# Performance work log

Hardware: AMD Instinct MI355X
Metric: run time of the kernel (lower is better)

The kernel has to match this reference:

```python
import jax, jax.numpy as jnp
import numpy as np

WS = 16      # window_size
OWS = 24     # overlap_win_size = int(16*0.5) + 16
PAD = 4      # (OWS - WS) // 2
NH = 6       # num_heads
DIM = 192
MLP_HID = 384  # dim * mlp_ratio(2)
TABLE = (WS + OWS - 1) ** 2  # 1521


def _ln(x, g, b, eps=1e-5):
    m = x.mean(-1, keepdims=True)
    v = ((x - m) ** 2).mean(-1, keepdims=True)
    return (x - m) * jax.lax.rsqrt(v + eps) * g + b


def setup_inputs() -> dict:
    key = jax.random.key(0)
    ks = jax.random.split(key, 16)
    B, H, W, C = 1, 192, 192, DIM
    x = jax.random.normal(ks[0], (B, H * W, C), jnp.float32)
    rpi = jax.random.randint(ks[1], (WS * WS, OWS * OWS), 0, TABLE, dtype=jnp.int64)
    s = 0.02
    return {
        "x": x,
        "rpi": rpi,
        "h": H,
        "w": W,
        "norm1_g": jnp.ones((C,), jnp.float32),
        "norm1_b": jnp.zeros((C,), jnp.float32),
        "qkv_w": jax.random.normal(ks[2], (C, 3 * C), jnp.float32) * s,
        "qkv_b": jnp.zeros((3 * C,), jnp.float32),
        "rpb_table": jax.random.normal(ks[3], (TABLE, NH), jnp.float32) * s,
        "proj_w": jax.random.normal(ks[4], (C, C), jnp.float32) * s,
        "proj_b": jnp.zeros((C,), jnp.float32),
        "norm2_g": jnp.ones((C,), jnp.float32),
        "norm2_b": jnp.zeros((C,), jnp.float32),
        "fc1_w": jax.random.normal(ks[5], (C, MLP_HID), jnp.float32) * s,
        "fc1_b": jnp.zeros((MLP_HID,), jnp.float32),
        "fc2_w": jax.random.normal(ks[6], (MLP_HID, C), jnp.float32) * s,
        "fc2_b": jnp.zeros((C,), jnp.float32),
    }


def reference(x, rpi, h, w, norm1_g, norm1_b, qkv_w, qkv_b, rpb_table,
              proj_w, proj_b, norm2_g, norm2_b, fc1_w, fc1_b, fc2_w, fc2_b):
    B, L, C = x.shape
    d = C // NH
    scale = d ** -0.5
    nhw, nww = h // WS, w // WS
    nW = nhw * nww

    shortcut = x
    xn = _ln(x, norm1_g, norm1_b).reshape(B, h, w, C)
    qkv = xn @ qkv_w + qkv_b                       # (B, h, w, 3C)
    q, k, v = jnp.split(qkv, 3, axis=-1)

    # non-overlapping query windows: (B*nW, WS*WS, C)
    qw = q.reshape(B, nhw, WS, nww, WS, C).transpose(0, 1, 3, 2, 4, 5)
    qw = qw.reshape(B * nW, WS * WS, C)

    # overlapping key/value windows via padded gather (equiv. to nn.Unfold)
    ri = (jnp.arange(nhw) * WS)[:, None] + jnp.arange(OWS)[None, :]  # (nhw, OWS)
    ci = (jnp.arange(nww) * WS)[:, None] + jnp.arange(OWS)[None, :]  # (nww, OWS)

    def win(t):
        tp = jnp.pad(t, ((0, 0), (PAD, PAD), (PAD, PAD), (0, 0)))
        g = tp[:, ri[:, :, None, None], ci[None, None, :, :], :]     # (B,nhw,OWS,nww,OWS,C)
        return g.transpose(0, 1, 3, 2, 4, 5).reshape(B * nW, OWS * OWS, C)

    kw, vw = win(k), win(v)

    qh = qw.reshape(B * nW, WS * WS, NH, d).transpose(0, 2, 1, 3) * scale
    kh = kw.reshape(B * nW, OWS * OWS, NH, d).transpose(0, 2, 1, 3)
    vh = vw.reshape(B * nW, OWS * OWS, NH, d).transpose(0, 2, 1, 3)

    attn = jnp.einsum('bhqd,bhkd->bhqk', qh, kh)
    bias = rpb_table[rpi.reshape(-1)].reshape(WS * WS, OWS * OWS, NH)
    bias = bias.transpose(2, 0, 1)                 # (NH, nq, n)
    attn = jax.nn.softmax(attn + bias[None], axis=-1)
    out = jnp.einsum('bhqk,bhkd->bhqd', attn, vh)
    out = out.transpose(0, 2, 1, 3).reshape(B * nW, WS * WS, C)

    # window reverse
    xr = out.reshape(B, nhw, nww, WS, WS, C).transpose(0, 1, 3, 2, 4, 5)
    xr = xr.reshape(B, h * w, C)

    x2 = xr @ proj_w + proj_b + shortcut
    x3 = _ln(x2, norm2_g, norm2_b)
    mlp = jax.nn.gelu(x3 @ fc1_w + fc1_b, approximate=False) @ fc2_w + fc2_b
    return x2 + mlp
```

## Files before the change

### kernel.cpp

```cpp
#include <hip/hip_runtime.h>
#include <hip/hip_bf16.h>

#define NH 6
#define DIM 192
#define HW 192
#define M_TOK (HW*HW)
#define QSC 0.25503488f
#define L2E 1.4426950408889634f

typedef __attribute__((ext_vector_type(8))) __bf16 bf16x8;
typedef __attribute__((ext_vector_type(8))) short short8;
typedef __attribute__((ext_vector_type(4))) short s16x4;
typedef __attribute__((ext_vector_type(4))) float floatx4;

__device__ inline unsigned short f2bf(float f) {
    union { float f; unsigned int u; } v; v.f = f;
    unsigned int r = (v.u + 0x7FFFu + ((v.u >> 16) & 1u)) >> 16;
    return (unsigned short)r;
}
__device__ inline short f2bfh(float f) {
    __bf16 b = (__bf16)f;
    return __builtin_bit_cast(short, b);
}
__device__ inline float exp2fast(float x) {
#if __has_builtin(__builtin_amdgcn_exp2f)
    return __builtin_amdgcn_exp2f(x);
#else
    return exp2f(x);
#endif
}
__device__ inline floatx4 bf4f(s16x4 b) {
    floatx4 f;
    #pragma unroll
    for (int r = 0; r < 4; r++) {
        union { unsigned u; float f; } v;
        v.u = ((unsigned)(unsigned short)b[r]) << 16;
        f[r] = v.f;
    }
    return f;
}

__device__ inline floatx4 mfma16(short8 a, short8 b, floatx4 c) {
    return __builtin_amdgcn_mfma_f32_16x16x32_bf16(
        __builtin_bit_cast(bf16x8, a), __builtin_bit_cast(bf16x8, b), c, 0, 0, 0);
}

template <int OFF>
__device__ inline s16x4 tr16(unsigned addr) {
    s16x4 r;
    asm volatile("ds_read_b64_tr_b16 %0, %1 offset:%2"
                 : "=&v"(r) : "v"(addr), "i"(OFF));
    return r;
}
template <int OFF>
__device__ inline s16x4 tr16m(unsigned addr) {
    s16x4 r;
    asm volatile("ds_read_b64_tr_b16 %0, %1 offset:%2"
                 : "=&v"(r) : "v"(addr), "i"(OFF) : "memory");
    return r;
}
template <int N>
__device__ __forceinline__ void wait_lgkm() {
    asm volatile("s_waitcnt lgkmcnt(%0)" :: "i"(N) : "memory");
}
__device__ inline short8 cat8(s16x4 a, s16x4 b) {
    return __builtin_shufflevector(a, b, 0, 1, 2, 3, 4, 5, 6, 7);
}

__device__ __forceinline__ void gload16(const void* g, unsigned lds_off) {
    __builtin_amdgcn_global_load_lds(
        (const __attribute__((address_space(1))) unsigned int*)(uintptr_t)g,
        (__attribute__((address_space(3))) unsigned int*)(uintptr_t)lds_off,
        16, 0, 0);
}

__device__ __forceinline__ void btfrag_body(int id, const int* __restrict__ rpi,
                                            const float* __restrict__ table,
                                            unsigned short* __restrict__ btf) {
    int lane = id & 63;
    int t = id >> 6;
    int kt = t % 36; t /= 36;
    int qt = t & 15; int hh = t >> 4;
    int k = kt * 16 + (lane & 15);
    int qb = qt * 16 + (lane >> 4) * 4;
    s16x4 v;
    #pragma unroll
    for (int r = 0; r < 4; r++)
        v[r] = f2bfh(table[rpi[(qb + r) * 576 + k] * NH + hh] * L2E);
    *(s16x4*)&btf[(size_t)id * 4] = v;
}

__device__ __forceinline__ void wcast_rest_body(int i2, const float* __restrict__ projw,
                                                const float* __restrict__ fc1w,
                                                const float* __restrict__ fc2w,
                                                unsigned short* __restrict__ wt_proj,
                                                unsigned short* __restrict__ wt_fc1,
                                                unsigned short* __restrict__ wt_fc2) {
    if (i2 < 36864) {
        int n = i2 / 192, k = i2 - n * 192;
        wt_proj[i2] = f2bf(projw[k * 192 + n]);
    } else if (i2 < 110592) {
        int i = i2 - 36864;
        int n = i / 192, k = i - n * 192;
        wt_fc1[i] = f2bf(fc1w[k * 384 + n]);
    } else {
        int i = i2 - 110592;
        int n = i / 384, k = i - n * 384;
        wt_fc2[i] = f2bf(fc2w[k * 192 + n]);
    }
}

__global__ __launch_bounds__(256) void prep_kernel(
    const float* __restrict__ qkvw,
    const float* __restrict__ x, const float* __restrict__ n1g,
    const float* __restrict__ n1b,
    unsigned short* __restrict__ wt_qkv,
    unsigned short* __restrict__ xn) {
    int bid = blockIdx.x;
    if (bid < 432) {
        int id = bid * 256 + threadIdx.x;
        int n = id / 192, k = id - n * 192;
        wt_qkv[id] = f2bf(qkvw[k * 576 + n]);
    } else {
        int row = (bid - 432) * 4 + (threadIdx.x >> 6);
        int lane = threadIdx.x & 63;
        const float* r = x + (size_t)row * DIM;
        float x0 = r[lane], x1 = r[lane + 64], x2 = r[lane + 128];
        float s = x0 + x1 + x2;
        #pragma unroll
        for (int m = 32; m >= 1; m >>= 1) s += __shfl_xor(s, m);
        float mean = s * (1.f / 192.f);
        float d0 = x0 - mean, d1 = x1 - mean, d2 = x2 - mean;
        float v = d0 * d0 + d1 * d1 + d2 * d2;
        #pragma unroll
        for (int m = 32; m >= 1; m >>= 1) v += __shfl_xor(v, m);
        float rstd = rsqrtf(v * (1.f / 192.f) + 1e-5f);
        unsigned short* o = xn + (size_t)row * DIM;
        o[lane]       = f2bf(d0 * rstd * n1g[lane]       + n1b[lane]);
        o[lane + 64]  = f2bf(d1 * rstd * n1g[lane + 64]  + n1b[lane + 64]);
        o[lane + 128] = f2bf(d2 * rstd * n1g[lane + 128] + n1b[lane + 128]);
    }
}

template <int MODE, int KK>
__global__ __launch_bounds__(256, 4) void gemm_kernel(
    const unsigned short* __restrict__ A,
    const unsigned short* __restrict__ Wt,
    const float* __restrict__ bias,
    void* __restrict__ outp,
    int N,
    const int* __restrict__ rpi, const float* __restrict__ table,
    unsigned short* __restrict__ btf,
    const float* __restrict__ projw, const float* __restrict__ fc1w,
    const float* __restrict__ fc2w,
    unsigned short* __restrict__ wt_proj, unsigned short* __restrict__ wt_fc1,
    unsigned short* __restrict__ wt_fc2) {
    if (MODE == 0 && blockIdx.y >= 9) {
        int extra = (blockIdx.y - 9) * 288 + blockIdx.x;
        if (extra < 864) {
            btfrag_body(extra * 256 + threadIdx.x, rpi, table, btf);
        } else if (extra < 1584) {
            wcast_rest_body((extra - 864) * 256 + threadIdx.x,
                            projw, fc1w, fc2w, wt_proj, wt_fc1, wt_fc2);
        }
        return;
    }
    __shared__ __align__(16) short sAB[19968];
    constexpr int STAGES = KK / 96;
    int tid = threadIdx.x;
    int w = tid >> 6, lane = tid & 63;
    int bm = blockIdx.x, bn = blockIdx.y;
    int lr = lane & 15, h = lane >> 4;
    floatx4 acc[2][4];
    #pragma unroll
    for (int i = 0; i < 2; i++)
        #pragma unroll
        for (int j = 0; j < 4; j++) acc[i][j] = (floatx4){0.f, 0.f, 0.f, 0.f};

    unsigned ldsbase = (unsigned)(uintptr_t)&sAB[0];

    for (int s = 0; s < STAGES; s++) {
        if (s) __syncthreads();
        for (int W = w; W < 39; W += 4) {
            int o = W * 1024 + lane * 16;
            const unsigned short* src;
            if (o < 26624) {
                int r = o / 208;
                int c = (o - r * 208) >> 4; c = c < 12 ? c : 11;
                src = &A[(size_t)(bm * 128 + r) * KK + s * 96 + c * 8];
            } else {
                int o2 = o - 26624;
                int r = o2 / 208;
                int c = (o2 - r * 208) >> 4; c = c < 12 ? c : 11;
                src = &Wt[(size_t)(bn * 64 + r) * KK + s * 96 + c * 8];
            }
            gload16(src, ldsbase + (unsigned)(W * 1024));
        }
        __syncthreads();
        #pragma unroll
        for (int kk = 0; kk < 3; kk++) {
            int kc = (kk * 4 + h) * 8;
            short8 a0 = *(const short8*)&sAB[(w * 32 + lr) * 104 + kc];
            short8 a1 = *(const short8*)&sAB[(w * 32 + 16 + lr) * 104 + kc];
            short8 b0 = *(const short8*)&sAB[13312 + (lr) * 104 + kc];
            short8 b1 = *(const short8*)&sAB[13312 + (16 + lr) * 104 + kc];
            short8 b2 = *(const short8*)&sAB[13312 + (32 + lr) * 104 + kc];
            short8 b3 = *(const short8*)&sAB[13312 + (48 + lr) * 104 + kc];
            acc[0][0] = mfma16(a0, b0, acc[0][0]);
            acc[0][1] = mfma16(a0, b1, acc[0][1]);
            acc[0][2] = mfma16(a0, b2, acc[0][2]);
            acc[0][3] = mfma16(a0, b3, acc[0][3]);
            acc[1][0] = mfma16(a1, b0, acc[1][0]);
            acc[1][1] = mfma16(a1, b1, acc[1][1]);
            acc[1][2] = mfma16(a1, b2, acc[1][2]);
            acc[1][3] = mfma16(a1, b3, acc[1][3]);
        }
    }

    int rowbase = bm * 128 + w * 32 + h * 4;
    int colbase = bn * 64;
    #pragma unroll
    for (int mi = 0; mi < 2; mi++) {
        #pragma unroll
        for (int ni = 0; ni < 4; ni++) {
            int c = colbase + ni * 16 + lr;
            float bv = bias[c];
            #pragma unroll
            for (int j = 0; j < 4; j++) {
                int r = rowbase + mi * 16 + j;
                float v = acc[mi][ni][j] + bv;
                if (MODE == 0) {
                    int part = c / 192;
                    int rem = c - part * 192;
                    int hd = rem >> 5, d = rem & 31;
                    if (part == 0) v *= QSC;
                    ((unsigned short*)outp)[((size_t)(part * 6 + hd) * M_TOK + r) * 32 + d] = f2bf(v);
                }
            }
        }
    }
}

__global__ __launch_bounds__(256, 2) void mega_kernel(
    const unsigned short* __restrict__ Aop,
    const unsigned short* __restrict__ Wp,
    const unsigned short* __restrict__ W1,
    const unsigned short* __restrict__ W2,
    const float* __restrict__ pb,
    const float* __restrict__ b1,
    const float* __restrict__ b2f,
    const float* __restrict__ res,
    const float* __restrict__ g2, const float* __restrict__ bb2,
    float* __restrict__ outp) {
    __shared__ __align__(16) short sA[13312];
    __shared__ __align__(16) short sH[6656];
    __shared__ __align__(16) short sB[10240];
    int tid = threadIdx.x;
    int w = tid >> 6, lane = tid & 63;
    int bm = blockIdx.x;
    int lr = lane & 15, h = lane >> 4;
    int lrow0 = w * 16 + h * 4;
    int row0 = bm * 64 + lrow0;

    floatx4 x2a[12];
    #pragma unroll
    for (int t = 0; t < 12; t++) x2a[t] = (floatx4){0.f, 0.f, 0.f, 0.f};

    auto stageB = [&](const unsigned short* base, int stride) {
        unsigned ldsB = (unsigned)(uintptr_t)&sB[0];
        #pragma unroll
        for (int W = 0; W < 5; W++) {
            int Wc = W * 4 + w;
            int o = Wc * 1024 + lane * 16;
            int r = o / 208;
            int c = (o - r * 208) >> 4; c = c < 12 ? c : 11;
            if (r > 95) { r = 95; c = 11; }
            gload16(&base[r * stride + c * 8], ldsB + (unsigned)(Wc * 1024));
        }
    };

    {
        unsigned ldsA = (unsigned)(uintptr_t)&sA[0];
        for (int W = w; W < 26; W += 4) {
            int o = W * 1024 + lane * 16;
            int sl = o / 13312;
            int o2 = o - sl * 13312;
            int r = o2 / 208;
            int c = (o2 - r * 208) >> 4; c = c < 12 ? c : 11;
            int col = sl * 96 + c * 8;
            int hd = col >> 5, d = col & 31;
            gload16(&Aop[((size_t)hd * M_TOK + bm * 64 + r) * 32 + d],
                    ldsA + (unsigned)(W * 1024));
        }
    }

#define GEMM6(ACCBASE, SAPTR) { \
    _Pragma("unroll") for (int kk = 0; kk < 3; kk++) { int kc = (kk * 4 + h) * 8; \
        short8 a_ = *(const short8*)&(SAPTR)[(w * 16 + lr) * 104 + kc]; \
        _Pragma("unroll") for (int ni = 0; ni < 6; ni++) { \
            short8 b_ = *(const short8*)&sB[(ni * 16 + lr) * 104 + kc]; \
            x2a[(ACCBASE) + ni] = mfma16(a_, b_, x2a[(ACCBASE) + ni]); } } }

#define GEMMH(SAPTR) { \
    _Pragma("unroll") for (int kk = 0; kk < 3; kk++) { int kc = (kk * 4 + h) * 8; \
        short8 a_ = *(const short8*)&(SAPTR)[(w * 16 + lr) * 104 + kc]; \
        _Pragma("unroll") for (int ni = 0; ni < 6; ni++) { \
            short8 b_ = *(const short8*)&sB[(ni * 16 + lr) * 104 + kc]; \
            ha[ni] = mfma16(a_, b_, ha[ni]); } } }

    stageB(Wp, 192);
    __syncthreads();
    GEMM6(0, sA);
    __syncthreads(); stageB(Wp + 96, 192); __syncthreads();
    GEMM6(0, sA + 6656);
    __syncthreads(); stageB(Wp + 96 * 192, 192); __syncthreads();
    GEMM6(6, sA);
    __syncthreads(); stageB(Wp + 96 * 192 + 96, 192); __syncthreads();
    GEMM6(6, sA + 6656);

    {
        float s1[4] = {0.f, 0.f, 0.f, 0.f}, s2[4] = {0.f, 0.f, 0.f, 0.f};
        #pragma unroll
        for (int t = 0; t < 12; t++) {
            int c = t * 16 + lr;
            float bv = pb[c];
            #pragma unroll
            for (int j = 0; j < 4; j++) {
                size_t idx = (size_t)(row0 + j) * 192 + c;
                float v = x2a[t][j] + bv + res[idx];
                x2a[t][j] = v;
                s1[j] += v;
                s2[j] += v * v;
            }
        }
        #pragma unroll
        for (int mask = 1; mask <= 8; mask <<= 1) {
            #pragma unroll
            for (int j = 0; j < 4; j++) {
                s1[j] += __shfl_xor(s1[j], mask);
                s2[j] += __shfl_xor(s2[j], mask);
            }
        }
        float mean[4], rstd[4];
        #pragma unroll
        for (int j = 0; j < 4; j++) {
            mean[j] = s1[j] * (1.f / 192.f);
            float var = s2[j] * (1.f / 192.f) - mean[j] * mean[j];
            rstd[j] = rsqrtf(var + 1e-5f);
        }
        #pragma unroll
        for (int t = 0; t < 12; t++) {
            int c = t * 16 + lr;
            float gw = g2[c], bw = bb2[c];
            int slab = t / 6;
            int cc = c - slab * 96;
            #pragma unroll
            for (int j = 0; j < 4; j++) {
                float lnv = (x2a[t][j] - mean[j]) * rstd[j] * gw + bw;
                sA[slab * 6656 + (lrow0 + j) * 104 + cc] = f2bfh(lnv);
            }
        }
    }

    for (int q = 0; q < 4; q++) {
        floatx4 ha[6];
        #pragma unroll
        for (int ni = 0; ni < 6; ni++) ha[ni] = (floatx4){0.f, 0.f, 0.f, 0.f};

        __syncthreads(); stageB(W1 + (size_t)(q * 96) * 192, 192); __syncthreads();
        GEMMH(sA);
        __syncthreads(); stageB(W1 + (size_t)(q * 96) * 192 + 96, 192); __syncthreads();
        GEMMH(sA + 6656);

        #pragma unroll
        for (int ni = 0; ni < 6; ni++) {
            int c384 = q * 96 + ni * 16 + lr;
            float bv = b1[c384];
            #pragma unroll
            for (int j = 0; j < 4; j++) {
                float v = ha[ni][j] + bv;
                float gl = 0.5f * v * (1.f + erff(v * 0.70710678118654752f));
                sH[(lrow0 + j) * 104 + ni * 16 + lr] = f2bfh(gl);
            }
        }

        __syncthreads(); stageB(W2 + q * 96, 384); __syncthreads();
        GEMM6(0, sH);
        __syncthreads(); stageB(W2 + (size_t)96 * 384 + q * 96, 384); __syncthreads();
        GEMM6(6, sH);
    }
#undef GEMM6
#undef GEMMH

    #pragma unroll
    for (int t = 0; t < 12; t++) {
        int c = t * 16 + lr;
        float bv = b2f[c];
        #pragma unroll
        for (int j = 0; j < 4; j++) {
            size_t idx = (size_t)(row0 + j) * 192 + c;
            outp[idx] = x2a[t][j] + bv;
        }
    }
}

__global__ __launch_bounds__(256, 3) void attn_mfma_kernel(
    const unsigned short* __restrict__ qkv,
    const unsigned short* __restrict__ btf,
    unsigned short* __restrict__ out) {
    __shared__ __align__(16) short sK[2][2304];
    __shared__ __align__(16) short sV[2][2048];
    __shared__ __align__(16) short sPt[4][4096];
    int win = blockIdx.x, head = blockIdx.y;
    int iy = win / 12, ix = win % 12;
    int tid = threadIdx.x;
    int w = tid >> 6, lane = tid & 63;
    int m = lane & 15, h = lane >> 4;

    const unsigned short* Qp = qkv + (size_t)head * M_TOK * 32;
    const unsigned short* Kp = qkv + (size_t)(6 + head) * M_TOK * 32;

    short8 qf[4];
    #pragma unroll
    for (int i = 0; i < 4; i++) {
        int wy = w * 4 + i;
        size_t tok = (size_t)(iy * 16 + wy) * HW + ix * 16 + m;
        qf[i] = *(const short8*)&Qp[tok * 32 + h * 8];
    }

    short ob = (m == 0) ? (short)0x3F80 : (short)0;
    short8 bones = {ob, ob, ob, ob, ob, ob, ob, ob};

    floatx4 oacc[4][2];
    floatx4 lacc[4];
    #pragma unroll
    for (int i = 0; i < 4; i++) {
        lacc[i] = (floatx4){0.f, 0.f, 0.f, 0.f};
        oacc[i][0] = (floatx4){0.f, 0.f, 0.f, 0.f};
        oacc[i][1] = (floatx4){0.f, 0.f, 0.f, 0.f};
    }

    int skey = tid >> 2, dq = tid & 3;
    short* kdst = &sK[0][skey * 36 + dq * 8];
    short* vdst = &sV[0][(dq >> 1) * 1024 + (skey >> 2) * 64 + (skey & 3) * 16 + (dq & 1) * 8];

    auto fetch = [&](int c, short8& kv, short8& vv) {
        int key = c * 64 + skey;
        int oy = key / 24, ox = key - (key / 24) * 24;
        int gy = iy * 16 - 4 + oy, gx = ix * 16 - 4 + ox;
        kv = (short8){0,0,0,0,0,0,0,0};
        vv = (short8){0,0,0,0,0,0,0,0};
        if (gy >= 0 && gy < HW && gx >= 0 && gx < HW) {
            const unsigned short* p = &Kp[((size_t)gy * HW + gx) * 32 + dq * 8];
            kv = *(const short8*)p;
            vv = *(const short8*)(p + 6 * M_TOK * 32);
        }
    };

    {
        short8 kv, vv;
        fetch(0, kv, vv);
        *(short8*)kdst = kv;
        *(short8*)vdst = vv;
    }

    unsigned sPbase = (unsigned)(uintptr_t)&sPt[w][0];
    unsigned sPa = sPbase + 8 * m + 256 * h;
    unsigned sVa0 = (unsigned)(uintptr_t)&sV[0][0] + 8 * m + 256 * h;
    char* sPwb = (char*)&sPt[w][0] + 128 * (m >> 2) + 32 * (m & 3) + 8 * h;

    for (int c = 0; c < 9; c++) {
        __syncthreads();
        int cur = c & 1;
        short8 knx, vnx;
        bool more = (c < 8);
        if (more) fetch(c + 1, knx, vnx);

        const short* sKc = sK[cur];
        short8 kfrag[4];
        #pragma unroll
        for (int kt = 0; kt < 4; kt++)
            kfrag[kt] = *(const short8*)&sKc[(kt * 16 + m) * 36 + h * 8];

        const unsigned short* bb = btf + ((((size_t)head * 16 + w * 4) * 36 + c * 4) * 64 + lane) * 4;

        #pragma unroll
        for (int i = 0; i < 4; i++) {
            floatx4 s[4];
            #pragma unroll
            for (int kt = 0; kt < 4; kt++)
                s[kt] = bf4f(*(const s16x4*)&bb[(size_t)(i * 36 + kt) * 256]);
            #pragma unroll
            for (int kt = 0; kt < 4; kt++)
                s[kt] = mfma16(qf[i], kfrag[kt], s[kt]);
            #pragma unroll
            for (int kt = 0; kt < 4; kt++) {
                s16x4 pk;
                #pragma unroll
                for (int r = 0; r < 4; r++)
                    pk[r] = f2bfh(exp2fast(s[kt][r]));
                *(s16x4*)(sPwb + i * 2048 + kt * 512) = pk;
            }
        }

        unsigned sVa = sVa0 + cur * 4096;
        short8 vb[4];
        {
            s16x4 lo0 = tr16<0>(sVa),    hi0 = tr16<128>(sVa);
            s16x4 lo1 = tr16<2048>(sVa), hi1 = tr16<2176>(sVa);
            s16x4 lo2 = tr16<1024>(sVa), hi2 = tr16<1152>(sVa);
            s16x4 lo3 = tr16<3072>(sVa), hi3 = tr16<3200>(sVa);
            vb[0] = cat8(lo0, hi0);
            vb[1] = cat8(lo1, hi1);
            vb[2] = cat8(lo2, hi2);
            vb[3] = cat8(lo3, hi3);
        }
        s16x4 pl0 = tr16m<0>(sPa),    ph0 = tr16m<128>(sPa);
        s16x4 pl1 = tr16m<1024>(sPa), ph1 = tr16m<1152>(sPa);
        #pragma unroll
        for (int i = 0; i < 4; i++) {
            s16x4 nl0, nh0, nl1, nh1;
            if (i < 3) {
                unsigned a = sPa + (unsigned)((i + 1) * 2048);
                nl0 = tr16m<0>(a);    nh0 = tr16m<128>(a);
                nl1 = tr16m<1024>(a); nh1 = tr16m<1152>(a);
                wait_lgkm<4>();
            } else {
                wait_lgkm<0>();
            }
            __builtin_amdgcn_sched_barrier(0);
            short8 pa0 = cat8(pl0, ph0);
            short8 pa1 = cat8(pl1, ph1);
            oacc[i][0] = mfma16(pa0, vb[0], oacc[i][0]);
            oacc[i][1] = mfma16(pa0, vb[1], oacc[i][1]);
            oacc[i][0] = mfma16(pa1, vb[2], oacc[i][0]);
            oacc[i][1] = mfma16(pa1, vb[3], oacc[i][1]);
            lacc[i] = mfma16(pa0, bones, lacc[i]);
            lacc[i] = mfma16(pa1, bones, lacc[i]);
            if (i < 3) { pl0 = nl0; ph0 = nh0; pl1 = nl1; ph1 = nh1; }
        }

        if (more) {
            int nb = 1 - cur;
            *(short8*)(kdst + nb * 2304) = knx;
            *(short8*)(vdst + nb * 2048) = vnx;
        }
    }

    unsigned short* Op = out + (size_t)head * M_TOK * 32;
    #pragma unroll
    for (int i = 0; i < 4; i++) {
        float inv[4];
        #pragma unroll
        for (int r = 0; r < 4; r++) {
            float sum = __shfl(lacc[i][r], lane & 48);
            inv[r] = 1.f / sum;
        }
        int wy = w * 4 + i;
        #pragma unroll
        for (int dt = 0; dt < 2; dt++)
            #pragma unroll
            for (int r = 0; r < 4; r++) {
                size_t tok = (size_t)(iy * 16 + wy) * HW + ix * 16 + h * 4 + r;
                Op[tok * 32 + dt * 16 + m] = f2bf(oacc[i][dt][r] * inv[r]);
            }
    }
}

extern "C" void kernel_launch(void* const* d_in, const int* in_sizes, int n_in,
                              void* d_out, int out_size, void* d_ws, size_t ws_size,
                              hipStream_t stream) {
    const float* x     = (const float*)d_in[0];
    const int*   rpi   = (const int*)d_in[1];
    const float* n1g   = (const float*)d_in[4];
    const float* n1b   = (const float*)d_in[5];
    const float* qkvw  = (const float*)d_in[6];
    const float* qkvb  = (const float*)d_in[7];
    const float* rpb   = (const float*)d_in[8];
    const float* projw = (const float*)d_in[9];
    const float* projb = (const float*)d_in[10];
    const float* n2g   = (const float*)d_in[11];
    const float* n2b   = (const float*)d_in[12];
    const float* fc1w  = (const float*)d_in[13];
    const float* fc1b  = (const float*)d_in[14];
    const float* fc2w  = (const float*)d_in[15];
    const float* fc2b  = (const float*)d_in[16];

    char* ws = (char*)d_ws;
    unsigned short* wt_qkv  = (unsigned short*)ws;
    unsigned short* wt_proj = wt_qkv + 110592;
    unsigned short* wt_fc1  = wt_proj + 36864;
    unsigned short* wt_fc2  = wt_fc1 + 73728;
    unsigned short* btf     = (unsigned short*)(ws + 589824);
    unsigned short* xn      = (unsigned short*)(ws + 4128768);
    unsigned short* qkv     = (unsigned short*)(ws + 18284544);
    unsigned short* attn_o  = (unsigned short*)(ws + 60751872);

    prep_kernel<<<9648, 256, 0, stream>>>(qkvw, x, n1g, n1b, wt_qkv, xn);
    gemm_kernel<0, 192><<<dim3(288, 15), 256, 0, stream>>>(
        xn, wt_qkv, qkvb, qkv, 576,
        rpi, rpb, btf, projw, fc1w, fc2w, wt_proj, wt_fc1, wt_fc2);
    attn_mfma_kernel<<<dim3(144, 6), 256, 0, stream>>>(qkv, btf, attn_o);
    mega_kernel<<<576, 256, 0, stream>>>(
        attn_o, wt_proj, wt_fc1, wt_fc2, projb, fc1b, fc2b,
        x, n2g, n2b, (float*)d_out);
}
```

Measured before the change: 154.1 us.

## Register-prefetch weight tiles in mega kernel with smaller tiles and higher occupancy

Replaces the direct global-to-LDS staging of weight tiles in the fused proj/LN/MLP kernel with a register double-buffer. The next tile is loaded into registers while the current tile is computed, and the old two-barrier-per-stage pattern is replaced by raw barriers and explicit waitcnts. Weight tiles shrink from 96 to 64 output columns, the MLP hidden loop is regrouped into 6 chunks of 64, and LDS is reduced so launch bounds can go from 2 to 3 blocks per CU. This aims to hide global load latency and raise occupancy, at the cost of more register pressure and more careful, error-prone synchronisation.

```diff
diff --git a/kernel.cpp b/kernel.cpp
--- a/kernel.cpp
+++ b/kernel.cpp
@@ -62,6 +62,13 @@
 template <int N>
 __device__ __forceinline__ void wait_lgkm() {
     asm volatile("s_waitcnt lgkmcnt(%0)" :: "i"(N) : "memory");
+}
+template <int N>
+__device__ __forceinline__ void wait_vm() {
+    asm volatile("s_waitcnt vmcnt(%0)" :: "i"(N) : "memory");
+}
+__device__ __forceinline__ void bar_raw() {
+    asm volatile("s_barrier" ::: "memory");
 }
 __device__ inline short8 cat8(s16x4 a, s16x4 b) {
     return __builtin_shufflevector(a, b, 0, 1, 2, 3, 4, 5, 6, 7);
@@ -241,7 +248,7 @@
     }
 }
 
-__global__ __launch_bounds__(256, 2) void mega_kernel(
+__global__ __launch_bounds__(256, 3) void mega_kernel(
     const unsigned short* __restrict__ Aop,
     const unsigned short* __restrict__ Wp,
     const unsigned short* __restrict__ W1,
@@ -253,8 +260,8 @@
     const float* __restrict__ g2, const float* __restrict__ bb2,
     float* __restrict__ outp) {
     __shared__ __align__(16) short sA[13312];
-    __shared__ __align__(16) short sH[6656];
-    __shared__ __align__(16) short sB[10240];
+    __shared__ __align__(16) short sH[4608];
+    __shared__ __align__(16) short sB[6656];
     int tid = threadIdx.x;
     int w = tid >> 6, lane = tid & 63;
     int bm = blockIdx.x;
@@ -266,18 +273,77 @@
     #pragma unroll
     for (int t = 0; t < 12; t++) x2a[t] = (floatx4){0.f, 0.f, 0.f, 0.f};
 
-    auto stageB = [&](const unsigned short* base, int stride) {
-        unsigned ldsB = (unsigned)(uintptr_t)&sB[0];
-        #pragma unroll
-        for (int W = 0; W < 5; W++) {
-            int Wc = W * 4 + w;
-            int o = Wc * 1024 + lane * 16;
-            int r = o / 208;
-            int c = (o - r * 208) >> 4; c = c < 12 ? c : 11;
-            if (r > 95) { r = 95; c = 11; }
-            gload16(&base[r * stride + c * 8], ldsB + (unsigned)(Wc * 1024));
+    short8 rg0, rg1, rg2;
+    auto loadreg96 = [&](const unsigned short* base) {
+        #pragma unroll
+        for (int k = 0; k < 3; k++) {
+            int d = (k * 256 + tid) * 16;
+            int r = d / 192, cc = (d - r * 192) >> 1;
+            short8 v = *(const short8*)&base[r * 192 + cc];
+            if (k == 0) rg0 = v; else if (k == 1) rg1 = v; else rg2 = v;
         }
     };
+    auto write96 = [&]() {
+        #pragma unroll
+        for (int k = 0; k < 3; k++) {
+            int d = (k * 256 + tid) * 16;
+            int r = d / 192, cc = (d - r * 192) >> 1;
+            *(short8*)&sB[r * 104 + cc] = (k == 0) ? rg0 : (k == 1) ? rg1 : rg2;
+        }
+    };
+    auto loadreg64 = [&](const unsigned short* base) {
+        #pragma unroll
+        for (int k = 0; k < 2; k++) {
+            int d = (k * 256 + tid) * 16;
+            int r = d / 128, cc = (d - r * 128) >> 1;
+            short8 v = *(const short8*)&base[r * 384 + cc];
+            if (k == 0) rg0 = v; else rg1 = v;
+        }
+    };
+    auto write64 = [&]() {
+        #pragma unroll
+        for (int k = 0; k < 2; k++) {
+            int d = (k * 256 + tid) * 16;
+            int r = d / 128, cc = (d - r * 128) >> 1;
+            *(short8*)&sB[r * 72 + cc] = (k == 0) ? rg0 : rg1;
+        }
+    };
+
+    auto comp96 = [&](floatx4* acc, const short* Ap) {
+        #pragma unroll
+        for (int kk = 0; kk < 3; kk++) {
+            int kc = (kk * 4 + h) * 8;
+            short8 a = *(const short8*)&Ap[(w * 16 + lr) * 104 + kc];
+            #pragma unroll
+            for (int ni = 0; ni < 4; ni++) {
+                short8 b = *(const short8*)&sB[(ni * 16 + lr) * 104 + kc];
+                acc[ni] = mfma16(a, b, acc[ni]);
+            }
+        }
+    };
+    auto comp64 = [&](floatx4* acc) {
+        #pragma unroll
+        for (int kk = 0; kk < 2; kk++) {
+            int kc = (kk * 4 + h) * 8;
+            short8 a = *(const short8*)&sH[(w * 16 + lr) * 72 + kc];
+            #pragma unroll
+            for (int ni = 0; ni < 4; ni++) {
+                short8 b = *(const short8*)&sB[(ni * 16 + lr) * 72 + kc];
+                acc[ni] = mfma16(a, b, acc[ni]);
+            }
+        }
+    };
+
+#define SCH __builtin_amdgcn_sched_barrier(0)
+#define ST96(LOADER, ACC, AP) \
+    bar_raw(); wait_vm<0>(); SCH; write96(); LOADER; wait_lgkm<0>(); SCH; \
+    bar_raw(); comp96(ACC, AP);
+#define ST96F(LOADER, ACC, AP) \
+    wait_vm<0>(); SCH; write96(); LOADER; wait_lgkm<0>(); SCH; \
+    bar_raw(); comp96(ACC, AP);
+#define ST64(LOADER, ACC) \
+    bar_raw(); wait_vm<0>(); SCH; write64(); LOADER; wait_lgkm<0>(); SCH; \
+    bar_raw(); comp64(ACC);
 
     {
         unsigned ldsA = (unsigned)(uintptr_t)&sA[0];
@@ -293,30 +359,14 @@
                     ldsA + (unsigned)(W * 1024));
         }
     }
-
-#define GEMM6(ACCBASE, SAPTR) { \
-    _Pragma("unroll") for (int kk = 0; kk < 3; kk++) { int kc = (kk * 4 + h) * 8; \
-        short8 a_ = *(const short8*)&(SAPTR)[(w * 16 + lr) * 104 + kc]; \
-        _Pragma("unroll") for (int ni = 0; ni < 6; ni++) { \
-            short8 b_ = *(const short8*)&sB[(ni * 16 + lr) * 104 + kc]; \
-            x2a[(ACCBASE) + ni] = mfma16(a_, b_, x2a[(ACCBASE) + ni]); } } }
-
-#define GEMMH(SAPTR) { \
-    _Pragma("unroll") for (int kk = 0; kk < 3; kk++) { int kc = (kk * 4 + h) * 8; \
-        short8 a_ = *(const short8*)&(SAPTR)[(w * 16 + lr) * 104 + kc]; \
-        _Pragma("unroll") for (int ni = 0; ni < 6; ni++) { \
-            short8 b_ = *(const short8*)&sB[(ni * 16 + lr) * 104 + kc]; \
-            ha[ni] = mfma16(a_, b_, ha[ni]); } } }
-
-    stageB(Wp, 192);
-    __syncthreads();
-    GEMM6(0, sA);
-    __syncthreads(); stageB(Wp + 96, 192); __syncthreads();
-    GEMM6(0, sA + 6656);
-    __syncthreads(); stageB(Wp + 96 * 192, 192); __syncthreads();
-    GEMM6(6, sA);
-    __syncthreads(); stageB(Wp + 96 * 192 + 96, 192); __syncthreads();
-    GEMM6(6, sA + 6656);
+    loadreg96(Wp);
+
+    ST96F(loadreg96(Wp + 64 * 192),        &x2a[0], sA);
+    ST96(loadreg96(Wp + 128 * 192),        &x2a[4], sA);
+    ST96(loadreg96(Wp + 96),               &x2a[8], sA);
+    ST96(loadreg96(Wp + 64 * 192 + 96),    &x2a[0], sA + 6656);
+    ST96(loadreg96(Wp + 128 * 192 + 96),   &x2a[4], sA + 6656);
+    ST96(loadreg96(W1),                    &x2a[8], sA + 6656);
 
     {
         float s1[4] = {0.f, 0.f, 0.f, 0.f}, s2[4] = {0.f, 0.f, 0.f, 0.f};
@@ -362,35 +412,38 @@
         }
     }
 
-    for (int q = 0; q < 4; q++) {
-        floatx4 ha[6];
-        #pragma unroll
-        for (int ni = 0; ni < 6; ni++) ha[ni] = (floatx4){0.f, 0.f, 0.f, 0.f};
-
-        __syncthreads(); stageB(W1 + (size_t)(q * 96) * 192, 192); __syncthreads();
-        GEMMH(sA);
-        __syncthreads(); stageB(W1 + (size_t)(q * 96) * 192 + 96, 192); __syncthreads();
-        GEMMH(sA + 6656);
-
-        #pragma unroll
-        for (int ni = 0; ni < 6; ni++) {
-            int c384 = q * 96 + ni * 16 + lr;
-            float bv = b1[c384];
+    for (int hg = 0; hg < 6; hg++) {
+        floatx4 ha[4];
+        #pragma unroll
+        for (int ni = 0; ni < 4; ni++) ha[ni] = (floatx4){0.f, 0.f, 0.f, 0.f};
+
+        ST96(loadreg96(W1 + (size_t)(hg * 64) * 192 + 96), ha, sA);
+        ST96(loadreg64(W2 + hg * 64),                      ha, sA + 6656);
+
+        #pragma unroll
+        for (int ni = 0; ni < 4; ni++) {
+            int hc = hg * 64 + ni * 16 + lr;
+            float bv = b1[hc];
             #pragma unroll
             for (int j = 0; j < 4; j++) {
                 float v = ha[ni][j] + bv;
                 float gl = 0.5f * v * (1.f + erff(v * 0.70710678118654752f));
-                sH[(lrow0 + j) * 104 + ni * 16 + lr] = f2bfh(gl);
-            }
-        }
-
-        __syncthreads(); stageB(W2 + q * 96, 384); __syncthreads();
-        GEMM6(0, sH);
-        __syncthreads(); stageB(W2 + (size_t)96 * 384 + q * 96, 384); __syncthreads();
-        GEMM6(6, sH);
-    }
-#undef GEMM6
-#undef GEMMH
+                sH[(lrow0 + j) * 72 + ni * 16 + lr] = f2bfh(gl);
+            }
+        }
+
+        ST64(loadreg64(W2 + (size_t)64 * 384 + hg * 64),  &x2a[0]);
+        ST64(loadreg64(W2 + (size_t)128 * 384 + hg * 64), &x2a[4]);
+        if (hg < 5) {
+            ST64(loadreg96(W1 + (size_t)((hg + 1) * 64) * 192), &x2a[8]);
+        } else {
+            ST64(, &x2a[8]);
+        }
+    }
+#undef ST96
+#undef ST96F
+#undef ST64
+#undef SCH
 
     #pragma unroll
     for (int t = 0; t < 12; t++) {
```

Result: faster. 130.6 us (median of 2 runs) (-15.3%).
